# Kernel tuning notes

Hardware: AMD Instinct MI355X
Metric: run time of the kernel (lower is better)

The kernel has to match this reference:

```python
import jax, jax.numpy as jnp
import numpy as np

N = 100000
E = 1600000
IN_FEATS = 256
HIDDEN = 128
CLASSES = 40

def _glorot(key, fan_in, fan_out):
    lim = float(np.sqrt(6.0 / (fan_in + fan_out)))
    return jax.random.uniform(key, (fan_in, fan_out), jnp.float32, -lim, lim)

def setup_inputs() -> dict:
    key = jax.random.key(0)
    ks = jax.random.split(key, 8)
    x = jax.random.normal(ks[0], (N, IN_FEATS), jnp.float32)
    src = jax.random.randint(ks[1], (E,), 0, N, jnp.int32)
    dst = jax.random.randint(ks[2], (E,), 0, N, jnp.int32)
    W0 = _glorot(ks[3], IN_FEATS, HIDDEN)
    b0 = jnp.zeros((HIDDEN,), jnp.float32)
    W1 = _glorot(ks[4], HIDDEN, HIDDEN)
    b1 = jnp.zeros((HIDDEN,), jnp.float32)
    Wc = _glorot(ks[5], HIDDEN, CLASSES)
    bc = jnp.zeros((CLASSES,), jnp.float32)
    return {"x": x, "src": src, "dst": dst, "W0": W0, "b0": b0,
            "W1": W1, "b1": b1, "Wc": Wc, "bc": bc}

def _degree_norms(src, dst, n):
    ones = jnp.ones(src.shape[0], jnp.float32)
    out_deg = jax.ops.segment_sum(ones, src, num_segments=n)
    in_deg = jax.ops.segment_sum(ones, dst, num_segments=n)
    c_src = jax.lax.rsqrt(jnp.maximum(out_deg, 1.0))  # D_out^{-1/2}
    c_dst = jax.lax.rsqrt(jnp.maximum(in_deg, 1.0))   # D_in^{-1/2}
    return c_src, c_dst

def _graph_conv(h, src, dst, c_src, c_dst, W, b, n):
    # transform first (cheaper when widths shrink), math-equivalent to DGL norm='both'
    h = h @ W
    h = h * c_src[:, None]
    agg = jax.ops.segment_sum(h[src], dst, num_segments=n)  # spmm gather/scatter
    return agg * c_dst[:, None] + b

def reference(x, src, dst, W0, b0, W1, b1, Wc, bc):
    n = x.shape[0]
    c_src, c_dst = _degree_norms(src, dst, n)
    h = _graph_conv(x, src, dst, c_src, c_dst, W0, b0, n)
    h = jax.nn.relu(h)  # dropout is identity at eval
    h = _graph_conv(h, src, dst, c_src, c_dst, W1, b1, n)
    logits = jax.nn.relu(h) @ Wc + bc
    return (h, logits)
```

## Files before the change

### kernel.cpp

```cpp
#include <hip/hip_runtime.h>
#include <cstdint>
#include <cstddef>


#define NPB 128
#define BSHIFT 7
#define EPT3 25
#define CHUNK (EPT3 * 256)

typedef __attribute__((ext_vector_type(8))) short short8;
typedef __attribute__((ext_vector_type(4))) float f32x4;

static __device__ __forceinline__ float4 ld4(const float* p) { return *(const float4*)p; }

static __device__ __forceinline__ float bf2f(unsigned int u) {
  union { unsigned int i; float f; } x; x.i = u << 16; return x.f;
}
static __device__ __forceinline__ unsigned int f2bf(float f) {
  union { float f; unsigned int i; } x; x.f = f;
  unsigned int r = x.i + 0x7fff + ((x.i >> 16) & 1);
  return r >> 16;
}

__global__ __launch_bounds__(256) void hist_prep(
    const int* __restrict__ src, const int* __restrict__ dst,
    const float* __restrict__ W0, const float* __restrict__ W1,
    ushort* __restrict__ W0t, ushort* __restrict__ W1t,
    int* __restrict__ bhD, int* __restrict__ bhS, int E, int nbk, int nblk) {
  __shared__ int hD[1024], hS[1024];
  int bid = blockIdx.x, t = threadIdx.x;
  if (bid >= nblk) {
    int idx = (bid - nblk) * 256 + t;
    if (idx < 128 * 256) {
      int nn = idx >> 8, kk = idx & 255;
      W0t[nn * 256 + kk] = (ushort)f2bf(W0[kk * 128 + nn]);
    }
    if (idx < 128 * 128) {
      int nn = idx >> 7, kk = idx & 127;
      W1t[nn * 128 + kk] = (ushort)f2bf(W1[kk * 128 + nn]);
    }
    return;
  }
  for (int i = t; i < nbk; i += 256) { hD[i] = 0; hS[i] = 0; }
  __syncthreads();
  int base = bid * CHUNK + t;
  for (int j = 0; j < EPT3; j++) {
    int e = base + j * 256;
    if (e < E) {
      atomicAdd(&hD[dst[e] >> BSHIFT], 1);
      atomicAdd(&hS[src[e] >> BSHIFT], 1);
    }
  }
  __syncthreads();
  for (int i = t; i < nbk; i += 256) {
    bhD[(size_t)bid * nbk + i] = hD[i];
    bhS[(size_t)bid * nbk + i] = hS[i];
  }
}

__global__ __launch_bounds__(256) void bucket_scan_blocks(int* __restrict__ bhD,
                                                          int* __restrict__ bhS,
                                                          int* __restrict__ totD,
                                                          int* __restrict__ totS,
                                                          int nbk, int nblk) {
  __shared__ int lds[256];
  int b = blockIdx.x, t = threadIdx.x;
  int v = (t < nblk) ? bhD[(size_t)t * nbk + b] : 0;
  lds[t] = v;
  __syncthreads();
  for (int off = 1; off < 256; off <<= 1) {
    int u = (t >= off) ? lds[t - off] : 0;
    __syncthreads();
    lds[t] += u;
    __syncthreads();
  }
  if (t < nblk) bhD[(size_t)t * nbk + b] = lds[t] - v;
  if (t == 255) totD[b] = lds[255];
  __syncthreads();
  int w = (t < nblk) ? bhS[(size_t)t * nbk + b] : 0;
  lds[t] = w;
  __syncthreads();
  for (int off = 1; off < 256; off <<= 1) {
    int u = (t >= off) ? lds[t - off] : 0;
    __syncthreads();
    lds[t] += u;
    __syncthreads();
  }
  if (t < nblk) bhS[(size_t)t * nbk + b] = lds[t] - w;
  if (t == 255) totS[b] = lds[255];
}

__global__ __launch_bounds__(1024) void bucket_base(const int* __restrict__ totD,
                                                    const int* __restrict__ totS,
                                                    int* __restrict__ baseD,
                                                    int* __restrict__ baseS, int nbk) {
  __shared__ int lds[1024];
  int t = threadIdx.x;
  int v = (t < nbk) ? totD[t] : 0;
  lds[t] = v;
  __syncthreads();
  for (int off = 1; off < 1024; off <<= 1) {
    int u = (t >= off) ? lds[t - off] : 0;
    __syncthreads();
    lds[t] += u;
    __syncthreads();
  }
  if (t < nbk) baseD[t] = lds[t] - v;
  if (t == 1023) baseD[nbk] = lds[1023];
  __syncthreads();
  int w = (t < nbk) ? totS[t] : 0;
  lds[t] = w;
  __syncthreads();
  for (int off = 1; off < 1024; off <<= 1) {
    int u = (t >= off) ? lds[t - off] : 0;
    __syncthreads();
    lds[t] += u;
    __syncthreads();
  }
  if (t < nbk) baseS[t] = lds[t] - w;
  if (t == 1023) baseS[nbk] = lds[1023];
}

__global__ __launch_bounds__(256) void bucket_scatter(
    const int* __restrict__ src, const int* __restrict__ dst,
    const int* __restrict__ bhD, const int* __restrict__ bhS,
    const int* __restrict__ baseD, const int* __restrict__ baseS,
    unsigned int* __restrict__ ebufD, uint8_t* __restrict__ ebufS,
    int E, int nbk) {
  __shared__ int cD[1024], cS[1024];
  int k = blockIdx.x, t = threadIdx.x;
  for (int i = t; i < nbk; i += 256) {
    cD[i] = baseD[i] + bhD[(size_t)k * nbk + i];
    cS[i] = baseS[i] + bhS[(size_t)k * nbk + i];
  }
  __syncthreads();
  int base = k * CHUNK + t;
  for (int j = 0; j < EPT3; j++) {
    int e = base + j * 256;
    if (e < E) {
      int s = src[e], d = dst[e];
      int pD = atomicAdd(&cD[d >> BSHIFT], 1);
      ebufD[pD] = ((unsigned int)(d & (NPB - 1)) << 17) | (unsigned int)s;
      int pS = atomicAdd(&cS[s >> BSHIFT], 1);
      ebufS[pS] = (uint8_t)(s & (NPB - 1));
    }
  }
}

__global__ __launch_bounds__(256) void csr_outdeg(
    const unsigned int* __restrict__ ebufD, const uint8_t* __restrict__ ebufS,
    const int* __restrict__ baseD, const int* __restrict__ baseS,
    int* __restrict__ row_start, int* __restrict__ csr,
    float* __restrict__ c_src, int n, int nbk) {
  __shared__ int cnt[NPB], sc[NPB], cur[NPB], cntS[NPB];
  int b = blockIdx.x, t = threadIdx.x;
  if (t < NPB) { cnt[t] = 0; cntS[t] = 0; }
  __syncthreads();
  int s0 = baseD[b], s1 = baseD[b + 1];
  for (int i = s0 + t; i < s1; i += 256) atomicAdd(&cnt[ebufD[i] >> 17], 1);
  int u0 = baseS[b], u1 = baseS[b + 1];
  for (int i = u0 + t; i < u1; i += 256) atomicAdd(&cntS[ebufS[i]], 1);
  __syncthreads();
  int c = (t < NPB) ? cnt[t] : 0;
  if (t < NPB) sc[t] = c;
  __syncthreads();
  for (int off = 1; off < NPB; off <<= 1) {
    int u = (t < NPB && t >= off) ? sc[t - off] : 0;
    __syncthreads();
    if (t < NPB) sc[t] += u;
    __syncthreads();
  }
  if (t < NPB) {
    int start = s0 + sc[t] - c;
    cur[t] = start;
    int node = b * NPB + t;
    if (node < n) {
      row_start[node] = start;
      c_src[node] = rsqrtf(fmaxf((float)cntS[t], 1.0f));
    }
  }
  if (b == 0 && t == 0) row_start[n] = baseD[nbk];
  __syncthreads();
  for (int i = s0 + t; i < s1; i += 256) {
    unsigned int wv = ebufD[i];
    int p = atomicAdd(&cur[wv >> 17], 1);
    csr[p] = (int)(wv & 0x1FFFFu);
  }
}

__global__ __launch_bounds__(256) void gemm256_mfma(const float* __restrict__ x,
                                                    const ushort* __restrict__ W0t,
                                                    const float* __restrict__ c_src,
                                                    ushort* __restrict__ t0b, int n) {
  __shared__ alignas(16) ushort As[64 * 64];
  __shared__ alignas(16) ushort Bs[128 * 64];
  int tid = threadIdx.x;
  int row0 = blockIdx.x * 64;
  int lane = tid & 63;
  int w = tid >> 6;
  int l16 = lane & 15, hi = lane >> 4;
  f32x4 acc[8];
#pragma unroll
  for (int c = 0; c < 8; c++) acc[c] = (f32x4){0.f, 0.f, 0.f, 0.f};

  for (int kt = 0; kt < 256; kt += 64) {
    {
      int r = tid >> 2;
      int gr = row0 + r;
#pragma unroll
      for (int u = 0; u < 2; u++) {
        int c8 = (tid & 3) * 2 + u;
        float4 v0 = make_float4(0.f, 0.f, 0.f, 0.f), v1 = v0;
        if (gr < n) {
          v0 = ld4(&x[(size_t)gr * 256 + kt + c8 * 8]);
          v1 = ld4(&x[(size_t)gr * 256 + kt + c8 * 8 + 4]);
        }
        uint4 o;
        o.x = f2bf(v0.x) | (f2bf(v0.y) << 16);
        o.y = f2bf(v0.z) | (f2bf(v0.w) << 16);
        o.z = f2bf(v1.x) | (f2bf(v1.y) << 16);
        o.w = f2bf(v1.z) | (f2bf(v1.w) << 16);
        *(uint4*)&As[r * 64 + (c8 ^ (r & 7)) * 8] = o;
      }
    }
    {
      int r = tid >> 1;
#pragma unroll
      for (int u = 0; u < 4; u++) {
        int c8 = (tid & 1) * 4 + u;
        uint4 o = *(const uint4*)&W0t[(size_t)r * 256 + kt + c8 * 8];
        *(uint4*)&Bs[r * 64 + (c8 ^ (r & 7)) * 8] = o;
      }
    }
    __syncthreads();
#pragma unroll
    for (int ks = 0; ks < 2; ks++) {
      int ar = w * 16 + l16;
      int ac = ks * 4 + hi;
      short8 a = *(const short8*)&As[ar * 64 + (ac ^ (ar & 7)) * 8];
#pragma unroll
      for (int c = 0; c < 8; c++) {
        int br = c * 16 + l16;
        short8 b = *(const short8*)&Bs[br * 64 + (ac ^ (br & 7)) * 8];
        acc[c] = __builtin_amdgcn_mfma_f32_16x16x32_bf16(a, b, acc[c], 0, 0, 0);
      }
    }
    __syncthreads();
  }
  float cs[4];
#pragma unroll
  for (int r = 0; r < 4; r++) {
    int gm = row0 + w * 16 + hi * 4 + r;
    cs[r] = (gm < n) ? c_src[gm] : 0.f;
  }
#pragma unroll
  for (int c = 0; c < 8; c++)
#pragma unroll
    for (int r = 0; r < 4; r++) {
      int gm = row0 + w * 16 + hi * 4 + r;
      if (gm < n) t0b[(size_t)gm * 128 + c * 16 + l16] = (ushort)f2bf(acc[c][r] * cs[r]);
    }
}

template <int MODE>
__global__ __launch_bounds__(256) void agg_kernel(const ushort* __restrict__ T,
                                                  const int* __restrict__ row_start,
                                                  const int* __restrict__ csr_src,
                                                  const float* __restrict__ c_src,
                                                  const float* __restrict__ bias,
                                                  unsigned int* __restrict__ out, int n) {
  int lane = threadIdx.x & 63;
  int gw = (blockIdx.x * 256 + threadIdx.x) >> 6;
  int nw = gridDim.x * 4;
  float bx = 0.f, by = 0.f;
  if (MODE == 0) { bx = bias[lane * 2]; by = bias[lane * 2 + 1]; }
  for (int node = gw; node < n; node += nw) {
    int e0 = row_start[node], e1 = row_start[node + 1];
    float ax = 0.f, ay = 0.f;
    for (int eb = e0; eb < e1; eb += 64) {
      int rem = e1 - eb;
      int cnt = rem < 64 ? rem : 64;
      int msrc = (lane < rem) ? csr_src[eb + lane] : 0;
      int j = 0;
      for (; j + 7 < cnt; j += 8) {
        unsigned int w[8];
#pragma unroll
        for (int u = 0; u < 8; u++) {
          int s = __shfl(msrc, j + u);
          w[u] = *(const unsigned int*)&T[(size_t)s * 128 + lane * 2];
        }
#pragma unroll
        for (int u = 0; u < 8; u++) {
          ax += bf2f(w[u] & 0xffff);
          ay += bf2f(w[u] >> 16);
        }
      }
      for (; j + 1 < cnt; j += 2) {
        int s0 = __shfl(msrc, j), s1 = __shfl(msrc, j + 1);
        unsigned int w0 = *(const unsigned int*)&T[(size_t)s0 * 128 + lane * 2];
        unsigned int w1 = *(const unsigned int*)&T[(size_t)s1 * 128 + lane * 2];
        ax += bf2f(w0 & 0xffff) + bf2f(w1 & 0xffff);
        ay += bf2f(w0 >> 16) + bf2f(w1 >> 16);
      }
      if (j < cnt) {
        int s0 = __shfl(msrc, j);
        unsigned int w0 = *(const unsigned int*)&T[(size_t)s0 * 128 + lane * 2];
        ax += bf2f(w0 & 0xffff);
        ay += bf2f(w0 >> 16);
      }
    }
    float cd = rsqrtf(fmaxf((float)(e1 - e0), 1.0f));
    float rx, ry;
    if (MODE == 0) {
      float csn = c_src[node];
      rx = fmaxf(fmaf(ax, cd, bx), 0.f) * csn;
      ry = fmaxf(fmaf(ay, cd, by), 0.f) * csn;
    } else {
      rx = ax * cd;
      ry = ay * cd;
    }
    out[(size_t)node * 64 + lane] = f2bf(rx) | (f2bf(ry) << 16);
  }
}

#define HSTRIDE 130
__global__ __launch_bounds__(256) void final_kernel(const ushort* __restrict__ gb,
                                                    const ushort* __restrict__ W1t,
                                                    const float* __restrict__ b1,
                                                    const float* __restrict__ Wc,
                                                    const float* __restrict__ bc,
                                                    float* __restrict__ h_out,
                                                    float* __restrict__ logits, int n) {
  __shared__ alignas(16) union {
    struct { ushort As[64 * 64]; ushort Bs[128 * 64]; } g;
    float Wl[128 * 40];
  } sm;
  __shared__ ushort Hs[64 * HSTRIDE];
  int tid = threadIdx.x;
  int row0 = blockIdx.x * 64;
  int lane = tid & 63;
  int w = tid >> 6;
  int l16 = lane & 15, hi = lane >> 4;
  f32x4 acc[8];
#pragma unroll
  for (int c = 0; c < 8; c++) acc[c] = (f32x4){0.f, 0.f, 0.f, 0.f};

  for (int kt = 0; kt < 128; kt += 64) {
    {
      int r = tid >> 2;
      int gr = row0 + r;
#pragma unroll
      for (int u = 0; u < 2; u++) {
        int c8 = (tid & 3) * 2 + u;
        uint4 o = make_uint4(0u, 0u, 0u, 0u);
        if (gr < n) o = *(const uint4*)&gb[(size_t)gr * 128 + kt + c8 * 8];
        *(uint4*)&sm.g.As[r * 64 + (c8 ^ (r & 7)) * 8] = o;
      }
    }
    {
      int r = tid >> 1;
#pragma unroll
      for (int u = 0; u < 4; u++) {
        int c8 = (tid & 1) * 4 + u;
        uint4 o = *(const uint4*)&W1t[(size_t)r * 128 + kt + c8 * 8];
        *(uint4*)&sm.g.Bs[r * 64 + (c8 ^ (r & 7)) * 8] = o;
      }
    }
    __syncthreads();
#pragma unroll
    for (int ks = 0; ks < 2; ks++) {
      int ar = w * 16 + l16;
      int ac = ks * 4 + hi;
      short8 a = *(const short8*)&sm.g.As[ar * 64 + (ac ^ (ar & 7)) * 8];
#pragma unroll
      for (int c = 0; c < 8; c++) {
        int br = c * 16 + l16;
        short8 b = *(const short8*)&sm.g.Bs[br * 64 + (ac ^ (br & 7)) * 8];
        acc[c] = __builtin_amdgcn_mfma_f32_16x16x32_bf16(a, b, acc[c], 0, 0, 0);
      }
    }
    __syncthreads();
  }
#pragma unroll
  for (int c = 0; c < 8; c++) {
    int col = c * 16 + l16;
    float bb = b1[col];
#pragma unroll
    for (int r = 0; r < 4; r++) {
      int rl = w * 16 + hi * 4 + r;
      int gm = row0 + rl;
      float h2 = acc[c][r] + bb;
      if (gm < n) h_out[(size_t)gm * 128 + col] = h2;
      Hs[rl * HSTRIDE + col] = (ushort)f2bf(fmaxf(h2, 0.f));
    }
  }
  __syncthreads();
  for (int i = tid; i < 128 * 40; i += 256) sm.Wl[i] = Wc[i];
  __syncthreads();
  int cg = tid & 7;
#pragma unroll
  for (int pass = 0; pass < 2; pass++) {
    int rl = pass * 32 + (tid >> 3);
    int gm = row0 + rl;
    if (gm < n) {
      float a5[5] = {0.f, 0.f, 0.f, 0.f, 0.f};
      for (int k = 0; k < 128; k++) {
        float v = bf2f(Hs[rl * HSTRIDE + k]);
#pragma unroll
        for (int j = 0; j < 5; j++) a5[j] = fmaf(v, sm.Wl[k * 40 + cg * 5 + j], a5[j]);
      }
#pragma unroll
      for (int j = 0; j < 5; j++)
        logits[(size_t)gm * 40 + cg * 5 + j] = a5[j] + bc[cg * 5 + j];
    }
  }
}

extern "C" void kernel_launch(void* const* d_in, const int* in_sizes, int n_in,
                              void* d_out, int out_size, void* d_ws, size_t ws_size,
                              hipStream_t stream) {
  const float* x = (const float*)d_in[0];
  const int* src = (const int*)d_in[1];
  const int* dst = (const int*)d_in[2];
  const float* W0 = (const float*)d_in[3];
  const float* b0 = (const float*)d_in[4];
  const float* W1 = (const float*)d_in[5];
  const float* b1 = (const float*)d_in[6];
  const float* Wc = (const float*)d_in[7];
  const float* bc = (const float*)d_in[8];
  const int n = in_sizes[0] / 256;
  const int E = in_sizes[1];
  const int nbk = (n + NPB - 1) >> BSHIFT;
  const int nblk = (E + CHUNK - 1) / CHUNK;

  char* wsp = (char*)d_ws;
  auto alloc = [&](size_t bytes) -> char* {
    char* p = wsp;
    wsp += (bytes + 255) & ~(size_t)255;
    return p;
  };
  ushort* t0b = (ushort*)alloc((size_t)n * 128 * sizeof(ushort));
  ushort* h1s = (ushort*)alloc((size_t)n * 128 * sizeof(ushort));
  float* c_src = (float*)alloc((size_t)n * sizeof(float));
  ushort* W0t = (ushort*)alloc((size_t)128 * 256 * sizeof(ushort));
  ushort* W1t = (ushort*)alloc((size_t)128 * 128 * sizeof(ushort));
  int* bhD = (int*)alloc((size_t)nblk * nbk * sizeof(int));
  int* bhS = (int*)alloc((size_t)nblk * nbk * sizeof(int));
  int* totD = (int*)alloc((size_t)nbk * sizeof(int));
  int* totS = (int*)alloc((size_t)nbk * sizeof(int));
  int* baseD = (int*)alloc((size_t)(nbk + 1) * sizeof(int));
  int* baseS = (int*)alloc((size_t)(nbk + 1) * sizeof(int));
  unsigned int* ebufD = (unsigned int*)alloc((size_t)E * sizeof(unsigned int));
  uint8_t* ebufS = (uint8_t*)alloc((size_t)E);
  int* row_start = (int*)alloc((size_t)(n + 1) * sizeof(int));
  int* csr = (int*)alloc((size_t)E * sizeof(int));

  float* h_out = (float*)d_out;
  float* logits = h_out + (size_t)n * 128;

  hist_prep<<<nblk + 128, 256, 0, stream>>>(src, dst, W0, W1, W0t, W1t,
                                            bhD, bhS, E, nbk, nblk);
  bucket_scan_blocks<<<nbk, 256, 0, stream>>>(bhD, bhS, totD, totS, nbk, nblk);
  bucket_base<<<1, 1024, 0, stream>>>(totD, totS, baseD, baseS, nbk);
  bucket_scatter<<<nblk, 256, 0, stream>>>(src, dst, bhD, bhS, baseD, baseS,
                                           ebufD, ebufS, E, nbk);
  csr_outdeg<<<nbk, 256, 0, stream>>>(ebufD, ebufS, baseD, baseS,
                                      row_start, csr, c_src, n, nbk);
  gemm256_mfma<<<(n + 63) / 64, 256, 0, stream>>>(x, W0t, c_src, t0b, n);
  agg_kernel<0><<<2048, 256, 0, stream>>>(t0b, row_start, csr, c_src, b0,
                                          (unsigned int*)h1s, n);
  agg_kernel<1><<<2048, 256, 0, stream>>>(h1s, row_start, csr, c_src, b1,
                                          (unsigned int*)t0b, n);
  final_kernel<<<(n + 63) / 64, 256, 0, stream>>>(t0b, W1t, b1, Wc, bc,
                                                  h_out, logits, n);
}
```

Before: 451.9 us.

## Fuse layer-2 aggregation into final GEMM kernel and inline bucket base scan

The second aggregation pass is merged into the final kernel. Each 512-thread block gathers neighbour rows for its 64 nodes straight into LDS, then runs the MFMA GEMM and the classifier from there. This drops one kernel launch and the full bf16 intermediate write and read-back. The separate single-block bucket_base kernel is also removed: each bucket_scatter and csr_outdeg block now recomputes the exclusive scan of the bucket totals itself, trading redundant per-block work for fewer launches. The fused kernel does its gather with one block per 64 nodes, fewer concurrent nodes than the old grid-stride aggregation, which may hurt latency hiding on the random gathers.

```diff
diff --git a/kernel.cpp b/kernel.cpp
--- a/kernel.cpp
+++ b/kernel.cpp
@@ -20,6 +20,33 @@
   union { float f; unsigned int i; } x; x.f = f;
   unsigned int r = x.i + 0x7fff + ((x.i >> 16) & 1);
   return r >> 16;
+}
+
+static __device__ __forceinline__ void excl_scan(const int* __restrict__ g,
+                                                 int* arr, int* scanT, int nbk) {
+  int t = threadIdx.x;
+  int v[4]; int s = 0;
+#pragma unroll
+  for (int j = 0; j < 4; j++) {
+    int idx = t * 4 + j;
+    v[j] = (idx < nbk) ? g[idx] : 0;
+    s += v[j];
+  }
+  scanT[t] = s;
+  __syncthreads();
+  for (int off = 1; off < 256; off <<= 1) {
+    int u = (t >= off) ? scanT[t - off] : 0;
+    __syncthreads();
+    scanT[t] += u;
+    __syncthreads();
+  }
+  int run = scanT[t] - s;
+#pragma unroll
+  for (int j = 0; j < 4; j++) {
+    arr[t * 4 + j] = run;
+    run += v[j];
+  }
+  __syncthreads();
 }
 
 __global__ __launch_bounds__(256) void hist_prep(
@@ -90,48 +117,20 @@
   if (t == 255) totS[b] = lds[255];
 }
 
-__global__ __launch_bounds__(1024) void bucket_base(const int* __restrict__ totD,
-                                                    const int* __restrict__ totS,
-                                                    int* __restrict__ baseD,
-                                                    int* __restrict__ baseS, int nbk) {
-  __shared__ int lds[1024];
-  int t = threadIdx.x;
-  int v = (t < nbk) ? totD[t] : 0;
-  lds[t] = v;
-  __syncthreads();
-  for (int off = 1; off < 1024; off <<= 1) {
-    int u = (t >= off) ? lds[t - off] : 0;
-    __syncthreads();
-    lds[t] += u;
-    __syncthreads();
-  }
-  if (t < nbk) baseD[t] = lds[t] - v;
-  if (t == 1023) baseD[nbk] = lds[1023];
-  __syncthreads();
-  int w = (t < nbk) ? totS[t] : 0;
-  lds[t] = w;
-  __syncthreads();
-  for (int off = 1; off < 1024; off <<= 1) {
-    int u = (t >= off) ? lds[t - off] : 0;
-    __syncthreads();
-    lds[t] += u;
-    __syncthreads();
-  }
-  if (t < nbk) baseS[t] = lds[t] - w;
-  if (t == 1023) baseS[nbk] = lds[1023];
-}
-
 __global__ __launch_bounds__(256) void bucket_scatter(
     const int* __restrict__ src, const int* __restrict__ dst,
     const int* __restrict__ bhD, const int* __restrict__ bhS,
-    const int* __restrict__ baseD, const int* __restrict__ baseS,
+    const int* __restrict__ totD, const int* __restrict__ totS,
     unsigned int* __restrict__ ebufD, uint8_t* __restrict__ ebufS,
     int E, int nbk) {
+  __shared__ int bD[1024], bS[1024], scanT[256];
   __shared__ int cD[1024], cS[1024];
   int k = blockIdx.x, t = threadIdx.x;
+  excl_scan(totD, bD, scanT, nbk);
+  excl_scan(totS, bS, scanT, nbk);
   for (int i = t; i < nbk; i += 256) {
-    cD[i] = baseD[i] + bhD[(size_t)k * nbk + i];
-    cS[i] = baseS[i] + bhS[(size_t)k * nbk + i];
+    cD[i] = bD[i] + bhD[(size_t)k * nbk + i];
+    cS[i] = bS[i] + bhS[(size_t)k * nbk + i];
   }
   __syncthreads();
   int base = k * CHUNK + t;
@@ -149,16 +148,19 @@
 
 __global__ __launch_bounds__(256) void csr_outdeg(
     const unsigned int* __restrict__ ebufD, const uint8_t* __restrict__ ebufS,
-    const int* __restrict__ baseD, const int* __restrict__ baseS,
+    const int* __restrict__ totD, const int* __restrict__ totS,
     int* __restrict__ row_start, int* __restrict__ csr,
-    float* __restrict__ c_src, int n, int nbk) {
+    float* __restrict__ c_src, int n, int nbk, int E) {
+  __shared__ int bD[1024], bS[1024], scanT[256];
   __shared__ int cnt[NPB], sc[NPB], cur[NPB], cntS[NPB];
   int b = blockIdx.x, t = threadIdx.x;
+  excl_scan(totD, bD, scanT, nbk);
+  excl_scan(totS, bS, scanT, nbk);
   if (t < NPB) { cnt[t] = 0; cntS[t] = 0; }
   __syncthreads();
-  int s0 = baseD[b], s1 = baseD[b + 1];
+  int s0 = bD[b], s1 = (b + 1 < 1024) ? bD[b + 1] : E;
   for (int i = s0 + t; i < s1; i += 256) atomicAdd(&cnt[ebufD[i] >> 17], 1);
-  int u0 = baseS[b], u1 = baseS[b + 1];
+  int u0 = bS[b], u1 = (b + 1 < 1024) ? bS[b + 1] : E;
   for (int i = u0 + t; i < u1; i += 256) atomicAdd(&cntS[ebufS[i]], 1);
   __syncthreads();
   int c = (t < NPB) ? cnt[t] : 0;
@@ -179,7 +181,7 @@
       c_src[node] = rsqrtf(fmaxf((float)cntS[t], 1.0f));
     }
   }
-  if (b == 0 && t == 0) row_start[n] = baseD[nbk];
+  if (b == 0 && t == 0) row_start[n] = E;
   __syncthreads();
   for (int i = s0 + t; i < s1; i += 256) {
     unsigned int wv = ebufD[i];
@@ -262,7 +264,6 @@
     }
 }
 
-template <int MODE>
 __global__ __launch_bounds__(256) void agg_kernel(const ushort* __restrict__ T,
                                                   const int* __restrict__ row_start,
                                                   const int* __restrict__ csr_src,
@@ -272,8 +273,7 @@
   int lane = threadIdx.x & 63;
   int gw = (blockIdx.x * 256 + threadIdx.x) >> 6;
   int nw = gridDim.x * 4;
-  float bx = 0.f, by = 0.f;
-  if (MODE == 0) { bx = bias[lane * 2]; by = bias[lane * 2 + 1]; }
+  float bx = bias[lane * 2], by = bias[lane * 2 + 1];
   for (int node = gw; node < n; node += nw) {
     int e0 = row_start[node], e1 = row_start[node + 1];
     float ax = 0.f, ay = 0.f;
@@ -310,109 +310,129 @@
       }
     }
     float cd = rsqrtf(fmaxf((float)(e1 - e0), 1.0f));
-    float rx, ry;
-    if (MODE == 0) {
-      float csn = c_src[node];
-      rx = fmaxf(fmaf(ax, cd, bx), 0.f) * csn;
-      ry = fmaxf(fmaf(ay, cd, by), 0.f) * csn;
-    } else {
-      rx = ax * cd;
-      ry = ay * cd;
-    }
+    float csn = c_src[node];
+    float rx = fmaxf(fmaf(ax, cd, bx), 0.f) * csn;
+    float ry = fmaxf(fmaf(ay, cd, by), 0.f) * csn;
     out[(size_t)node * 64 + lane] = f2bf(rx) | (f2bf(ry) << 16);
   }
 }
 
 #define HSTRIDE 130
-__global__ __launch_bounds__(256) void final_kernel(const ushort* __restrict__ gb,
-                                                    const ushort* __restrict__ W1t,
-                                                    const float* __restrict__ b1,
-                                                    const float* __restrict__ Wc,
-                                                    const float* __restrict__ bc,
-                                                    float* __restrict__ h_out,
-                                                    float* __restrict__ logits, int n) {
+__global__ __launch_bounds__(512) void agg_final(
+    const ushort* __restrict__ h1s, const int* __restrict__ row_start,
+    const int* __restrict__ csr_src, const ushort* __restrict__ W1t,
+    const float* __restrict__ b1, const float* __restrict__ Wc,
+    const float* __restrict__ bc, float* __restrict__ h_out,
+    float* __restrict__ logits, int n) {
   __shared__ alignas(16) union {
-    struct { ushort As[64 * 64]; ushort Bs[128 * 64]; } g;
-    float Wl[128 * 40];
+    struct { ushort As[64 * 128]; ushort Bs[128 * 64]; } g;
+    struct { ushort Hs[64 * HSTRIDE]; float Wl[128 * 40]; } l;
   } sm;
-  __shared__ ushort Hs[64 * HSTRIDE];
   int tid = threadIdx.x;
-  int row0 = blockIdx.x * 64;
   int lane = tid & 63;
   int w = tid >> 6;
   int l16 = lane & 15, hi = lane >> 4;
-  f32x4 acc[8];
-#pragma unroll
-  for (int c = 0; c < 8; c++) acc[c] = (f32x4){0.f, 0.f, 0.f, 0.f};
-
+  int row0 = blockIdx.x * 64;
+
+  for (int i = 0; i < 8; i++) {
+    int rl = w * 8 + i;
+    int node = row0 + rl;
+    float ax = 0.f, ay = 0.f;
+    if (node < n) {
+      int e0 = row_start[node], e1 = row_start[node + 1];
+      for (int eb = e0; eb < e1; eb += 64) {
+        int rem = e1 - eb;
+        int cnt = rem < 64 ? rem : 64;
+        int msrc = (lane < rem) ? csr_src[eb + lane] : 0;
+        int j = 0;
+        for (; j + 7 < cnt; j += 8) {
+          unsigned int wv[8];
+#pragma unroll
+          for (int u = 0; u < 8; u++) {
+            int s = __shfl(msrc, j + u);
+            wv[u] = *(const unsigned int*)&h1s[(size_t)s * 128 + lane * 2];
+          }
+#pragma unroll
+          for (int u = 0; u < 8; u++) {
+            ax += bf2f(wv[u] & 0xffff);
+            ay += bf2f(wv[u] >> 16);
+          }
+        }
+        for (; j < cnt; j++) {
+          int s = __shfl(msrc, j);
+          unsigned int wv = *(const unsigned int*)&h1s[(size_t)s * 128 + lane * 2];
+          ax += bf2f(wv & 0xffff);
+          ay += bf2f(wv >> 16);
+        }
+      }
+      float cd = rsqrtf(fmaxf((float)(e1 - e0), 1.0f));
+      ax *= cd;
+      ay *= cd;
+    }
+    unsigned int pr = f2bf(ax) | (f2bf(ay) << 16);
+    int ch = lane >> 2;
+    *(unsigned int*)&sm.g.As[rl * 128 + ((ch ^ (rl & 7)) << 3) + ((lane & 3) << 1)] = pr;
+  }
+  __syncthreads();
+
+  int wr = w & 3, wc = w >> 2;
+  f32x4 acc[4];
+#pragma unroll
+  for (int c = 0; c < 4; c++) acc[c] = (f32x4){0.f, 0.f, 0.f, 0.f};
   for (int kt = 0; kt < 128; kt += 64) {
     {
       int r = tid >> 2;
-      int gr = row0 + r;
 #pragma unroll
       for (int u = 0; u < 2; u++) {
         int c8 = (tid & 3) * 2 + u;
-        uint4 o = make_uint4(0u, 0u, 0u, 0u);
-        if (gr < n) o = *(const uint4*)&gb[(size_t)gr * 128 + kt + c8 * 8];
-        *(uint4*)&sm.g.As[r * 64 + (c8 ^ (r & 7)) * 8] = o;
-      }
-    }
-    {
-      int r = tid >> 1;
-#pragma unroll
-      for (int u = 0; u < 4; u++) {
-        int c8 = (tid & 1) * 4 + u;
         uint4 o = *(const uint4*)&W1t[(size_t)r * 128 + kt + c8 * 8];
-        *(uint4*)&sm.g.Bs[r * 64 + (c8 ^ (r & 7)) * 8] = o;
+        *(uint4*)&sm.g.Bs[r * 64 + ((c8 ^ (r & 7)) << 3)] = o;
       }
     }
     __syncthreads();
 #pragma unroll
     for (int ks = 0; ks < 2; ks++) {
-      int ar = w * 16 + l16;
-      int ac = ks * 4 + hi;
-      short8 a = *(const short8*)&sm.g.As[ar * 64 + (ac ^ (ar & 7)) * 8];
-#pragma unroll
-      for (int c = 0; c < 8; c++) {
-        int br = c * 16 + l16;
-        short8 b = *(const short8*)&sm.g.Bs[br * 64 + (ac ^ (br & 7)) * 8];
+      int ar = wr * 16 + l16;
+      int ch = (kt >> 3) + ks * 4 + hi;
+      short8 a = *(const short8*)&sm.g.As[ar * 128 + ((ch ^ (ar & 7)) << 3)];
+#pragma unroll
+      for (int c = 0; c < 4; c++) {
+        int br = wc * 64 + c * 16 + l16;
+        short8 b = *(const short8*)&sm.g.Bs[br * 64 + (((ks * 4 + hi) ^ (br & 7)) << 3)];
         acc[c] = __builtin_amdgcn_mfma_f32_16x16x32_bf16(a, b, acc[c], 0, 0, 0);
       }
     }
     __syncthreads();
   }
-#pragma unroll
-  for (int c = 0; c < 8; c++) {
-    int col = c * 16 + l16;
+
+#pragma unroll
+  for (int c = 0; c < 4; c++) {
+    int col = wc * 64 + c * 16 + l16;
     float bb = b1[col];
 #pragma unroll
     for (int r = 0; r < 4; r++) {
-      int rl = w * 16 + hi * 4 + r;
+      int rl = wr * 16 + hi * 4 + r;
       int gm = row0 + rl;
       float h2 = acc[c][r] + bb;
       if (gm < n) h_out[(size_t)gm * 128 + col] = h2;
-      Hs[rl * HSTRIDE + col] = (ushort)f2bf(fmaxf(h2, 0.f));
-    }
-  }
-  __syncthreads();
-  for (int i = tid; i < 128 * 40; i += 256) sm.Wl[i] = Wc[i];
-  __syncthreads();
-  int cg = tid & 7;
-#pragma unroll
-  for (int pass = 0; pass < 2; pass++) {
-    int rl = pass * 32 + (tid >> 3);
-    int gm = row0 + rl;
-    if (gm < n) {
-      float a5[5] = {0.f, 0.f, 0.f, 0.f, 0.f};
-      for (int k = 0; k < 128; k++) {
-        float v = bf2f(Hs[rl * HSTRIDE + k]);
-#pragma unroll
-        for (int j = 0; j < 5; j++) a5[j] = fmaf(v, sm.Wl[k * 40 + cg * 5 + j], a5[j]);
-      }
-#pragma unroll
-      for (int j = 0; j < 5; j++)
-        logits[(size_t)gm * 40 + cg * 5 + j] = a5[j] + bc[cg * 5 + j];
-    }
+      sm.l.Hs[rl * HSTRIDE + col] = (ushort)f2bf(fmaxf(h2, 0.f));
+    }
+  }
+  for (int i = tid; i < 128 * 40; i += 512) sm.l.Wl[i] = Wc[i];
+  __syncthreads();
+
+  int rl = tid >> 3, cg = tid & 7;
+  int gm = row0 + rl;
+  if (gm < n) {
+    float a5[5] = {0.f, 0.f, 0.f, 0.f, 0.f};
+    for (int k = 0; k < 128; k++) {
+      float v = bf2f(sm.l.Hs[rl * HSTRIDE + k]);
+#pragma unroll
+      for (int j = 0; j < 5; j++) a5[j] = fmaf(v, sm.l.Wl[k * 40 + cg * 5 + j], a5[j]);
+    }
+#pragma unroll
+    for (int j = 0; j < 5; j++)
+      logits[(size_t)gm * 40 + cg * 5 + j] = a5[j] + bc[cg * 5 + j];
   }
 }
 
@@ -448,8 +468,6 @@
   int* bhS = (int*)alloc((size_t)nblk * nbk * sizeof(int));
   int* totD = (int*)alloc((size_t)nbk * sizeof(int));
   int* totS = (int*)alloc((size_t)nbk * sizeof(int));
-  int* baseD = (int*)alloc((size_t)(nbk + 1) * sizeof(int));
-  int* baseS = (int*)alloc((size_t)(nbk + 1) * sizeof(int));
   unsigned int* ebufD = (unsigned int*)alloc((size_t)E * sizeof(unsigned int));
   uint8_t* ebufS = (uint8_t*)alloc((size_t)E);
   int* row_start = (int*)alloc((size_t)(n + 1) * sizeof(int));
@@ -461,16 +479,13 @@
   hist_prep<<<nblk + 128, 256, 0, stream>>>(src, dst, W0, W1, W0t, W1t,
                                             bhD, bhS, E, nbk, nblk);
   bucket_scan_blocks<<<nbk, 256, 0, stream>>>(bhD, bhS, totD, totS, nbk, nblk);
-  bucket_base<<<1, 1024, 0, stream>>>(totD, totS, baseD, baseS, nbk);
-  bucket_scatter<<<nblk, 256, 0, stream>>>(src, dst, bhD, bhS, baseD, baseS,
+  bucket_scatter<<<nblk, 256, 0, stream>>>(src, dst, bhD, bhS, totD, totS,
                                            ebufD, ebufS, E, nbk);
-  csr_outdeg<<<nbk, 256, 0, stream>>>(ebufD, ebufS, baseD, baseS,
-                                      row_start, csr, c_src, n, nbk);
+  csr_outdeg<<<nbk, 256, 0, stream>>>(ebufD, ebufS, totD, totS,
+                                      row_start, csr, c_src, n, nbk, E);
   gemm256_mfma<<<(n + 63) / 64, 256, 0, stream>>>(x, W0t, c_src, t0b, n);
-  agg_kernel<0><<<2048, 256, 0, stream>>>(t0b, row_start, csr, c_src, b0,
-                                          (unsigned int*)h1s, n);
-  agg_kernel<1><<<2048, 256, 0, stream>>>(h1s, row_start, csr, c_src, b1,
-                                          (unsigned int*)t0b, n);
-  final_kernel<<<(n + 63) / 64, 256, 0, stream>>>(t0b, W1t, b1, Wc, bc,
-                                                  h_out, logits, n);
-}
+  agg_kernel<<<2048, 256, 0, stream>>>(t0b, row_start, csr, c_src, b0,
+                                       (unsigned int*)h1s, n);
+  agg_final<<<(n + 63) / 64, 512, 0, stream>>>(h1s, row_start, csr, W1t, b1,
+                                               Wc, bc, h_out, logits, n);
+}
```

New measurement: 446.7 us. No clear change (-1.1%).
